# Performance work log

Hardware: AMD Instinct MI355X
Metric: run time of the kernel (lower is better)

## Reference

```python
import jax, jax.numpy as jnp
import numpy as np

NVEC = [100000, 100000, 100000]
OFFSETS = np.concatenate([[0], np.cumsum(NVEC)[:-1]]).astype(np.int32)  # [0,100000,200000]
DIM = 64
B = 500000
HID = 50
IN_DIM = len(NVEC) * DIM + 1  # 193


def setup_inputs() -> dict:
    key = jax.random.key(0)
    ks = jax.random.split(key, 7)
    batch_ind = jax.random.randint(ks[0], (B, len(NVEC)), 0, NVEC[0], dtype=jnp.int32)
    batch_t = jax.random.uniform(ks[1], (B,), dtype=jnp.float32)
    U = jax.random.uniform(ks[2], (int(np.sum(NVEC)), DIM), dtype=jnp.float32)
    W1 = jax.random.normal(ks[3], (IN_DIM, HID), dtype=jnp.float32) * 0.1
    b1 = jax.random.normal(ks[4], (HID,), dtype=jnp.float32) * 0.1
    W2 = jax.random.normal(ks[5], (HID, 1), dtype=jnp.float32) * 0.1
    b2 = jax.random.normal(ks[6], (1,), dtype=jnp.float32) * 0.1
    return {"batch_ind": batch_ind, "batch_t": batch_t, "U": U,
            "W1": W1, "b1": b1, "W2": W2, "b2": b2}


def reference(batch_ind, batch_t, U, W1, b1, W2, b2):
    # per-mode gather: offset each mode's index into the concatenated U table
    offs = jnp.asarray(OFFSETS)  # [nmod]
    idx = batch_ind + offs[None, :]          # [B, nmod] global row ids
    emb = U[idx]                              # [B, nmod, D] single fused gather
    X = jnp.concatenate([emb.reshape(emb.shape[0], -1),
                         batch_t[:, None]], axis=1)  # [B, nmod*D+1]
    h = jnp.tanh(X @ W1 + b1)                 # [B, 50]
    return h @ W2 + b2                        # [B, 1]
```

## Files before the change

kernel.cpp:

```cpp
#include <hip/hip_runtime.h>
#include <hip/hip_bf16.h>

using bf16x8 = __attribute__((ext_vector_type(8))) short;
using f32x4  = __attribute__((ext_vector_type(4))) float;

#define THREADS 256
#define NBLOCKS 768
#define NTILES  31250

__device__ __forceinline__ short f2bf(float f) {
    unsigned u = __float_as_uint(f);
    unsigned r = (u + 0x7fffu + ((u >> 16) & 1u)) >> 16;
    return (short)r;
}

__device__ __forceinline__ bf16x8 cvt8(float4 a, float4 b) {
    bf16x8 r;
    r[0] = f2bf(a.x); r[1] = f2bf(a.y); r[2] = f2bf(a.z); r[3] = f2bf(a.w);
    r[4] = f2bf(b.x); r[5] = f2bf(b.y); r[6] = f2bf(b.z); r[7] = f2bf(b.w);
    return r;
}

__global__ __launch_bounds__(THREADS) void etl_kernel(
    const int*   __restrict__ bi,
    const float* __restrict__ t,
    const float* __restrict__ U,
    const float* __restrict__ W1,
    const float* __restrict__ b1,
    const float* __restrict__ W2,
    const float* __restrict__ b2,
    float*       __restrict__ out)
{
    __shared__ short bsh[24][64][8];
    for (int e = threadIdx.x; e < 24 * 64; e += THREADS) {
        int f = e >> 6, l = e & 63;
        int nt = f / 6, ks = f - nt * 6;
        int n  = nt * 16 + (l & 15);
        int k0 = ks * 32 + ((l >> 4) << 3);
        bf16x8 v;
#pragma unroll
        for (int j = 0; j < 8; ++j) {
            float w = (n < 50) ? W1[(k0 + j) * 50 + n] : 0.f;
            v[j] = f2bf(w);
        }
        *(bf16x8*)(&bsh[f][l][0]) = v;
    }
    __syncthreads();

    const int lane = threadIdx.x & 63;
    const int g    = lane >> 4;
    const int ncol = lane & 15;

    bf16x8 Bf[24];
#pragma unroll
    for (int f = 0; f < 24; ++f) Bf[f] = *(const bf16x8*)(&bsh[f][lane][0]);

    float w192[4], b1r[4], w2r[4];
#pragma unroll
    for (int nt = 0; nt < 4; ++nt) {
        int n = nt * 16 + ncol;
        bool vld = (n < 50);
        w192[nt] = vld ? W1[192 * 50 + n] : 0.f;
        b1r[nt]  = vld ? b1[n] : 0.f;
        w2r[nt]  = vld ? W2[n] : 0.f;
    }
    const float b2v = b2[0];

    const int nwaves = NBLOCKS * (THREADS / 64);
    const int wid    = blockIdx.x * (THREADS / 64) + (threadIdx.x >> 6);

    for (int tile = wid; tile < NTILES; tile += nwaves) {
        const int base = tile * 16;
        const int row  = base + ncol;

        int i0 = bi[row * 3 + 0];
        int i1 = bi[row * 3 + 1] + 100000;
        int i2 = bi[row * 3 + 2] + 200000;

        bf16x8 A[6];
        {
            const float* p0 = U + (size_t)i0 * 64 + g * 8;
            const float* p1 = U + (size_t)i1 * 64 + g * 8;
            const float* p2 = U + (size_t)i2 * 64 + g * 8;
            float4 a0 = ((const float4*)p0)[0], a1 = ((const float4*)p0)[1];
            float4 a2 = ((const float4*)(p0 + 32))[0], a3 = ((const float4*)(p0 + 32))[1];
            float4 b0 = ((const float4*)p1)[0], b1v4 = ((const float4*)p1)[1];
            float4 b2v4 = ((const float4*)(p1 + 32))[0], b3 = ((const float4*)(p1 + 32))[1];
            float4 c0 = ((const float4*)p2)[0], c1 = ((const float4*)p2)[1];
            float4 c2 = ((const float4*)(p2 + 32))[0], c3 = ((const float4*)(p2 + 32))[1];
            A[0] = cvt8(a0, a1);  A[1] = cvt8(a2, a3);
            A[2] = cvt8(b0, b1v4); A[3] = cvt8(b2v4, b3);
            A[4] = cvt8(c0, c1);  A[5] = cvt8(c2, c3);
        }

        f32x4 acc[4];
#pragma unroll
        for (int nt = 0; nt < 4; ++nt) acc[nt] = (f32x4){0.f, 0.f, 0.f, 0.f};

#pragma unroll
        for (int ks = 0; ks < 6; ++ks) {
#pragma unroll
            for (int nt = 0; nt < 4; ++nt) {
                acc[nt] = __builtin_amdgcn_mfma_f32_16x16x32_bf16(
                    A[ks], Bf[nt * 6 + ks], acc[nt], 0, 0, 0);
            }
        }

        float4 tv = *(const float4*)(t + base + g * 4);
        float tarr[4] = {tv.x, tv.y, tv.z, tv.w};
        float part[4] = {0.f, 0.f, 0.f, 0.f};
#pragma unroll
        for (int nt = 0; nt < 4; ++nt) {
#pragma unroll
            for (int r = 0; r < 4; ++r) {
                float pre = acc[nt][r] + tarr[r] * w192[nt] + b1r[nt];
                float e  = __expf(2.f * pre);
                float h  = 1.f - 2.f * __builtin_amdgcn_rcpf(e + 1.f);
                part[r] += h * w2r[nt];
            }
        }
#pragma unroll
        for (int r = 0; r < 4; ++r) {
#pragma unroll
            for (int m = 1; m < 16; m <<= 1)
                part[r] += __shfl_xor(part[r], m, 64);
        }
        if (ncol == 0) {
            float4 o = make_float4(part[0] + b2v, part[1] + b2v,
                                   part[2] + b2v, part[3] + b2v);
            *(float4*)(out + base + g * 4) = o;
        }
    }
}

extern "C" void kernel_launch(void* const* d_in, const int* in_sizes, int n_in,
                              void* d_out, int out_size, void* d_ws, size_t ws_size,
                              hipStream_t stream) {
    const int*   bi = (const int*)  d_in[0];
    const float* t  = (const float*)d_in[1];
    const float* U  = (const float*)d_in[2];
    const float* W1 = (const float*)d_in[3];
    const float* b1 = (const float*)d_in[4];
    const float* W2 = (const float*)d_in[5];
    const float* b2 = (const float*)d_in[6];
    float* out = (float*)d_out;
    etl_kernel<<<NBLOCKS, THREADS, 0, stream>>>(bi, t, U, W1, b1, W2, b2, out);
}
```

Measured before the change: 66.13 us.

## Read B fragments from LDS per tile to cut registers and raise occupancy

The 24 bf16x8 weight fragments and the epilogue constants are no longer held in registers for the whole kernel. They are re-read from shared memory inside each tile, which lowers VGPR pressure so launch_bounds can request 8 waves per SIMD. The grid grows from 768 to 2048 blocks to fill the extra occupancy. This should hide more gather latency, at the cost of extra LDS reads per tile and a repeated weight-staging prologue in each of the additional blocks. The manual bf16 rounding is also replaced with the library conversion.

```diff
diff --git a/kernel.cpp b/kernel.cpp
--- a/kernel.cpp
+++ b/kernel.cpp
@@ -5,13 +5,12 @@
 using f32x4  = __attribute__((ext_vector_type(4))) float;
 
 #define THREADS 256
-#define NBLOCKS 768
+#define NBLOCKS 2048
 #define NTILES  31250
 
 __device__ __forceinline__ short f2bf(float f) {
-    unsigned u = __float_as_uint(f);
-    unsigned r = (u + 0x7fffu + ((u >> 16) & 1u)) >> 16;
-    return (short)r;
+    __hip_bfloat16 h = __float2bfloat16(f);
+    return __builtin_bit_cast(short, h);
 }
 
 __device__ __forceinline__ bf16x8 cvt8(float4 a, float4 b) {
@@ -21,7 +20,7 @@
     return r;
 }
 
-__global__ __launch_bounds__(THREADS) void etl_kernel(
+__global__ __launch_bounds__(THREADS, 8) void etl_kernel(
     const int*   __restrict__ bi,
     const float* __restrict__ t,
     const float* __restrict__ U,
@@ -32,6 +31,9 @@
     float*       __restrict__ out)
 {
     __shared__ short bsh[24][64][8];
+    __shared__ float esh[3][4][16];
+    __shared__ float b2s;
+
     for (int e = threadIdx.x; e < 24 * 64; e += THREADS) {
         int f = e >> 6, l = e & 63;
         int nt = f / 6, ks = f - nt * 6;
@@ -45,26 +47,20 @@
         }
         *(bf16x8*)(&bsh[f][l][0]) = v;
     }
+    if (threadIdx.x < 192) {
+        int j = threadIdx.x >> 6, l = threadIdx.x & 63;
+        int nt = l >> 4, nc = l & 15;
+        int n = nt * 16 + nc;
+        float v = 0.f;
+        if (n < 50) v = (j == 0) ? W1[192 * 50 + n] : (j == 1) ? b1[n] : W2[n];
+        esh[j][nt][nc] = v;
+    }
+    if (threadIdx.x == 0) b2s = b2[0];
     __syncthreads();
 
     const int lane = threadIdx.x & 63;
     const int g    = lane >> 4;
     const int ncol = lane & 15;
-
-    bf16x8 Bf[24];
-#pragma unroll
-    for (int f = 0; f < 24; ++f) Bf[f] = *(const bf16x8*)(&bsh[f][lane][0]);
-
-    float w192[4], b1r[4], w2r[4];
-#pragma unroll
-    for (int nt = 0; nt < 4; ++nt) {
-        int n = nt * 16 + ncol;
-        bool vld = (n < 50);
-        w192[nt] = vld ? W1[192 * 50 + n] : 0.f;
-        b1r[nt]  = vld ? b1[n] : 0.f;
-        w2r[nt]  = vld ? W2[n] : 0.f;
-    }
-    const float b2v = b2[0];
 
     const int nwaves = NBLOCKS * (THREADS / 64);
     const int wid    = blockIdx.x * (THREADS / 64) + (threadIdx.x >> 6);
@@ -88,9 +84,9 @@
             float4 b2v4 = ((const float4*)(p1 + 32))[0], b3 = ((const float4*)(p1 + 32))[1];
             float4 c0 = ((const float4*)p2)[0], c1 = ((const float4*)p2)[1];
             float4 c2 = ((const float4*)(p2 + 32))[0], c3 = ((const float4*)(p2 + 32))[1];
-            A[0] = cvt8(a0, a1);  A[1] = cvt8(a2, a3);
+            A[0] = cvt8(a0, a1);   A[1] = cvt8(a2, a3);
             A[2] = cvt8(b0, b1v4); A[3] = cvt8(b2v4, b3);
-            A[4] = cvt8(c0, c1);  A[5] = cvt8(c2, c3);
+            A[4] = cvt8(c0, c1);   A[5] = cvt8(c2, c3);
         }
 
         f32x4 acc[4];
@@ -101,8 +97,9 @@
         for (int ks = 0; ks < 6; ++ks) {
 #pragma unroll
             for (int nt = 0; nt < 4; ++nt) {
+                bf16x8 Bf = *(const bf16x8*)(&bsh[nt * 6 + ks][lane][0]);
                 acc[nt] = __builtin_amdgcn_mfma_f32_16x16x32_bf16(
-                    A[ks], Bf[nt * 6 + ks], acc[nt], 0, 0, 0);
+                    A[ks], Bf, acc[nt], 0, 0, 0);
             }
         }
 
@@ -111,12 +108,15 @@
         float part[4] = {0.f, 0.f, 0.f, 0.f};
 #pragma unroll
         for (int nt = 0; nt < 4; ++nt) {
+            float w192 = esh[0][nt][ncol];
+            float b1r  = esh[1][nt][ncol];
+            float w2r  = esh[2][nt][ncol];
 #pragma unroll
             for (int r = 0; r < 4; ++r) {
-                float pre = acc[nt][r] + tarr[r] * w192[nt] + b1r[nt];
+                float pre = acc[nt][r] + tarr[r] * w192 + b1r;
                 float e  = __expf(2.f * pre);
                 float h  = 1.f - 2.f * __builtin_amdgcn_rcpf(e + 1.f);
-                part[r] += h * w2r[nt];
+                part[r] += h * w2r;
             }
         }
 #pragma unroll
@@ -126,6 +126,7 @@
                 part[r] += __shfl_xor(part[r], m, 64);
         }
         if (ncol == 0) {
+            float b2v = b2s;
             float4 o = make_float4(part[0] + b2v, part[1] + b2v,
                                    part[2] + b2v, part[3] + b2v);
             *(float4*)(out + base + g * 4) = o;
```

Result: slower. 101.7 us (+53.7%).
